# Performance work log

Measured on AMD Instinct MI355X. Metric: run time of the kernel, lower is better.

## Reference

```python
import jax, jax.numpy as jnp
import numpy as np

B, S, D, U = 8, 2048, 512, 512
L0, L1 = 128, 128  # limit_context (left, right)


def setup_inputs() -> dict:
    key = jax.random.key(0)
    ks = jax.random.split(key, 7)
    scale = 1.0 / np.sqrt(D).astype(np.float32)
    return {
        "x": jax.random.normal(ks[0], (B, S, D), dtype=jnp.float32),
        "Wq": jax.random.normal(ks[1], (D, U), dtype=jnp.float32) * scale,
        "Wk": jax.random.normal(ks[2], (D, U), dtype=jnp.float32) * scale,
        "Wv": jax.random.normal(ks[3], (D, U), dtype=jnp.float32) * scale,
        "bq": jnp.zeros((U,), dtype=jnp.float32),
        "bk": jnp.zeros((U,), dtype=jnp.float32),
        "bv": jnp.zeros((U,), dtype=jnp.float32),
    }


def reference(x, Wq, Wk, Wv, bq, bk, bv):
    # Linear projections for query / key / value (shared input x)
    q = x @ Wq + bq  # [B,S,U]
    k = x @ Wk + bk  # [B,S,U]
    v = x @ Wv + bv  # [B,S,U]

    inv_sqrt_dv = jnp.float32(1.0 / np.sqrt(U))
    scores = jnp.einsum("bqd,bkd->bqk", q, k) * inv_sqrt_dv  # [B,S,S]

    # Sliding-window mask: key j visible to query i iff i-L0 <= j <= i+L1.
    # Equivalent to the original per-step softmax over values[:, start:end].
    i = jnp.arange(S)[:, None]
    j = jnp.arange(S)[None, :]
    window = (j >= i - L0) & (j <= i + L1)  # [S,S]
    neg_inf = jnp.finfo(scores.dtype).min
    scores = jnp.where(window[None], scores, neg_inf)

    attn = jax.nn.softmax(scores, axis=-1)  # [B,S,S]
    return jnp.einsum("bqk,bkd->bqd", attn, v)  # [B,S,U]
```

## Files before the change

### kernel.cpp

```cpp
#include <hip/hip_runtime.h>

#define BATCH 8
#define S_LEN 2048
#define DDIM 512
#define UDIM 512
#define WIN_L 128
#define WIN_R 128

typedef _Float16 f16;
typedef __attribute__((ext_vector_type(8))) _Float16 f16x8;
typedef __attribute__((ext_vector_type(4))) _Float16 f16x4;
typedef __attribute__((ext_vector_type(4))) float f32x4;

__device__ __forceinline__ void gload_lds16(const void* g, void* l) {
  __builtin_amdgcn_global_load_lds((const __attribute__((address_space(1))) void*)g,
                                   (__attribute__((address_space(3))) void*)l, 16, 0, 0);
}

__global__ void cast_f32_f16(const float* __restrict__ in, f16* __restrict__ out, int n) {
  int i = (blockIdx.x * blockDim.x + threadIdx.x) * 4;
  if (i < n) {
    float4 v = *(const float4*)(in + i);
    f16x4 o;
    o[0] = (f16)v.x; o[1] = (f16)v.y; o[2] = (f16)v.z; o[3] = (f16)v.w;
    *(f16x4*)(out + i) = o;
  }
}

__global__ void transpose_w(const float* __restrict__ Wq, const float* __restrict__ Wk,
                            const float* __restrict__ Wv, f16* __restrict__ WT) {
  const float* W = blockIdx.z == 0 ? Wq : (blockIdx.z == 1 ? Wk : Wv);
  f16* WTz = WT + (size_t)blockIdx.z * DDIM * UDIM;
  __shared__ float t[32][33];
  int tx = threadIdx.x & 31, ty = threadIdx.x >> 5;
  int n0 = blockIdx.x * 32, k0 = blockIdx.y * 32;
  for (int i = 0; i < 4; i++) {
    int r = ty * 4 + i;
    t[r][tx] = W[(size_t)(k0 + r) * UDIM + n0 + tx];
  }
  __syncthreads();
  for (int i = 0; i < 4; i++) {
    int r = ty * 4 + i;
    WTz[(size_t)(n0 + r) * DDIM + k0 + tx] = (f16)t[tx][r];
  }
}

__global__ __launch_bounds__(256, 2) void gemm_qkv(
    const f16* __restrict__ X, const f16* __restrict__ WT,
    const float* __restrict__ bq, const float* __restrict__ bk, const float* __restrict__ bv,
    f16* __restrict__ QKV, f16* __restrict__ VT) {
  int z = blockIdx.z;
  const f16* WTz = WT + (size_t)z * DDIM * UDIM;
  const float* bias = z == 0 ? bq : (z == 1 ? bk : bv);
  f16* out = QKV + (size_t)z * (BATCH * S_LEN) * UDIM;

  __shared__ f16 Al[128 * 32];
  __shared__ f16 Bl[128 * 32];

  int tid = threadIdx.x, wv = tid >> 6, ln = tid & 63;
  int m0 = blockIdx.x * 128, n0 = blockIdx.y * 128;
  int wm = (wv >> 1) * 64, wn = (wv & 1) * 64;
  int lm = ln & 15, lq = ln >> 4;
  int srow = ln >> 2, scol = (ln & 3) * 8;

  f32x4 acc[4][4];
  for (int mt = 0; mt < 4; mt++)
    for (int nt = 0; nt < 4; nt++)
      for (int r = 0; r < 4; r++) acc[mt][nt][r] = 0.f;

  for (int k0 = 0; k0 < DDIM; k0 += 32) {
    for (int half = 0; half < 2; half++) {
      int r0 = half * 64 + wv * 16;
      gload_lds16(X + (size_t)(m0 + r0 + srow) * DDIM + k0 + scol, &Al[r0 * 32]);
      gload_lds16(WTz + (size_t)(n0 + r0 + srow) * DDIM + k0 + scol, &Bl[r0 * 32]);
    }
    __syncthreads();
    f16x8 af[4], bfr[4];
    for (int mt = 0; mt < 4; mt++) af[mt] = *(const f16x8*)&Al[(wm + mt * 16 + lm) * 32 + lq * 8];
    for (int nt = 0; nt < 4; nt++) bfr[nt] = *(const f16x8*)&Bl[(wn + nt * 16 + lm) * 32 + lq * 8];
    for (int mt = 0; mt < 4; mt++)
      for (int nt = 0; nt < 4; nt++)
        acc[mt][nt] = __builtin_amdgcn_mfma_f32_16x16x32_f16(af[mt], bfr[nt], acc[mt][nt], 0, 0, 0);
    __syncthreads();
  }

  if (z == 2) {
    for (int mt = 0; mt < 4; mt++)
      for (int nt = 0; nt < 4; nt++) {
        int col = n0 + wn + nt * 16 + lm;
        float bv_ = bias[col];
        int row0 = m0 + wm + mt * 16 + lq * 4;
        int bb = row0 >> 11, ss = row0 & 2047;
        f16x4 o;
        for (int r = 0; r < 4; r++) o[r] = (f16)(acc[mt][nt][r] + bv_);
        *(f16x4*)&VT[((size_t)bb * UDIM + col) * S_LEN + ss] = o;
      }
  } else {
    for (int mt = 0; mt < 4; mt++)
      for (int nt = 0; nt < 4; nt++) {
        int col = n0 + wn + nt * 16 + lm;
        float bv_ = bias[col];
        for (int r = 0; r < 4; r++) {
          int row = m0 + wm + mt * 16 + lq * 4 + r;
          out[(size_t)row * UDIM + col] = (f16)(acc[mt][nt][r] + bv_);
        }
      }
  }
}

__global__ __launch_bounds__(256, 2) void attn(
    const f16* __restrict__ Q, const f16* __restrict__ K, const f16* __restrict__ VT,
    float* __restrict__ out) {
  __shared__ float Sb[32 * 33];
  __shared__ f16 Pb[32 * 40];
  __shared__ float mrun[32], lrun[32], alph[32];

  int tid = threadIdx.x, wv = tid >> 6, ln = tid & 63;
  int lm = ln & 15, lq = ln >> 4;
  int b = blockIdx.x, q0 = blockIdx.y * 32;
  const size_t base = (size_t)b * S_LEN;

  if (tid < 32) { mrun[tid] = -INFINITY; lrun[tid] = 0.f; }

  int smt = wv >> 1, snt = wv & 1;
  f16x8 qf[16];
  {
    const f16* qrow = Q + (base + q0 + smt * 16 + lm) * (size_t)DDIM + lq * 8;
    for (int kk = 0; kk < 16; kk++) qf[kk] = *(const f16x8*)(qrow + kk * 32);
  }
  f32x4 oacc[2][8];
  for (int mt = 0; mt < 2; mt++)
    for (int nt = 0; nt < 8; nt++)
      for (int r = 0; r < 4; r++) oacc[mt][nt][r] = 0.f;

  int jlo = q0 - WIN_L; if (jlo < 0) jlo = 0;
  int jhi = q0 + 32 + WIN_R; if (jhi > S_LEN) jhi = S_LEN;

  const f16* krow = K + (base + snt * 16 + lm) * (size_t)DDIM + lq * 8;
  const f16* vrow = VT + ((size_t)b * UDIM + wv * 128 + lm) * S_LEN + lq * 8;
  const float scale = 0.044194173824159216f;

  for (int j0 = jlo; j0 < jhi; j0 += 32) {
    const f16* kp = krow + (size_t)j0 * DDIM;
    f32x4 sacc0, sacc1;
    for (int r = 0; r < 4; r++) { sacc0[r] = 0.f; sacc1[r] = 0.f; }
    for (int kk = 0; kk < 16; kk += 2) {
      f16x8 b0 = *(const f16x8*)(kp + kk * 32);
      f16x8 b1 = *(const f16x8*)(kp + (kk + 1) * 32);
      sacc0 = __builtin_amdgcn_mfma_f32_16x16x32_f16(qf[kk], b0, sacc0, 0, 0, 0);
      sacc1 = __builtin_amdgcn_mfma_f32_16x16x32_f16(qf[kk + 1], b1, sacc1, 0, 0, 0);
    }
    for (int r = 0; r < 4; r++) {
      int row = smt * 16 + lq * 4 + r;
      int col = snt * 16 + lm;
      int qi = q0 + row, kj = j0 + col;
      float v = (sacc0[r] + sacc1[r]) * scale;
      if (kj < qi - WIN_L || kj > qi + WIN_R) v = -INFINITY;
      Sb[row * 33 + col] = v;
    }
    __syncthreads();

    {
      int r = tid >> 3, l8 = tid & 7;
      float sv[4];
      float mx = -INFINITY;
      for (int cc = 0; cc < 4; cc++) {
        sv[cc] = Sb[r * 33 + l8 * 4 + cc];
        mx = fmaxf(mx, sv[cc]);
      }
      mx = fmaxf(mx, __shfl_xor(mx, 1));
      mx = fmaxf(mx, __shfl_xor(mx, 2));
      mx = fmaxf(mx, __shfl_xor(mx, 4));
      float mold = mrun[r];
      float mnew = fmaxf(mold, mx);
      float a = __expf(mold - mnew);
      float sum = 0.f;
      for (int cc = 0; cc < 4; cc++) {
        float p = __expf(sv[cc] - mnew);
        sum += p;
        Pb[r * 40 + l8 * 4 + cc] = (f16)p;
      }
      sum += __shfl_xor(sum, 1);
      sum += __shfl_xor(sum, 2);
      sum += __shfl_xor(sum, 4);
      if (l8 == 0) {
        lrun[r] = a * lrun[r] + sum;
        mrun[r] = mnew;
        alph[r] = a;
      }
    }
    __syncthreads();

    {
      float al[2][4];
      for (int mt = 0; mt < 2; mt++)
        for (int r = 0; r < 4; r++) al[mt][r] = alph[mt * 16 + lq * 4 + r];
      for (int mt = 0; mt < 2; mt++)
        for (int nt = 0; nt < 8; nt++)
          for (int r = 0; r < 4; r++) oacc[mt][nt][r] *= al[mt][r];
      f16x8 pf[2];
      for (int mt = 0; mt < 2; mt++)
        pf[mt] = *(const f16x8*)&Pb[(mt * 16 + lm) * 40 + lq * 8];
      const f16* vp = vrow + j0;
      for (int nt = 0; nt < 8; nt++) {
        f16x8 bfr = *(const f16x8*)(vp + (size_t)nt * 16 * S_LEN);
        oacc[0][nt] = __builtin_amdgcn_mfma_f32_16x16x32_f16(pf[0], bfr, oacc[0][nt], 0, 0, 0);
        oacc[1][nt] = __builtin_amdgcn_mfma_f32_16x16x32_f16(pf[1], bfr, oacc[1][nt], 0, 0, 0);
      }
    }
  }

  {
    float linv[2][4];
    for (int mt = 0; mt < 2; mt++)
      for (int r = 0; r < 4; r++) linv[mt][r] = 1.0f / lrun[mt * 16 + lq * 4 + r];
    for (int mt = 0; mt < 2; mt++)
      for (int nt = 0; nt < 8; nt++)
        for (int r = 0; r < 4; r++) {
          int row = q0 + mt * 16 + lq * 4 + r;
          int col = wv * 128 + nt * 16 + lm;
          out[(base + row) * (size_t)UDIM + col] = oacc[mt][nt][r] * linv[mt][r];
        }
  }
}

extern "C" void kernel_launch(void* const* d_in, const int* in_sizes, int n_in,
                              void* d_out, int out_size, void* d_ws, size_t ws_size,
                              hipStream_t stream) {
  const float* x  = (const float*)d_in[0];
  const float* Wq = (const float*)d_in[1];
  const float* Wk = (const float*)d_in[2];
  const float* Wv = (const float*)d_in[3];
  const float* bq = (const float*)d_in[4];
  const float* bk = (const float*)d_in[5];
  const float* bv = (const float*)d_in[6];
  float* out = (float*)d_out;

  char* ws = (char*)d_ws;
  const size_t XB_BYTES  = (size_t)BATCH * S_LEN * DDIM * 2;
  const size_t WT_BYTES  = (size_t)3 * DDIM * UDIM * 2;
  const size_t QKV_BYTES = (size_t)3 * BATCH * S_LEN * UDIM * 2;
  f16* xb  = (f16*)ws;
  f16* WT  = (f16*)(ws + XB_BYTES);
  f16* QKV = (f16*)(ws + XB_BYTES + WT_BYTES);
  f16* VT  = (f16*)(ws + XB_BYTES + WT_BYTES + QKV_BYTES);

  int n = BATCH * S_LEN * DDIM;
  cast_f32_f16<<<n / (256 * 4), 256, 0, stream>>>(x, xb, n);
  transpose_w<<<dim3(16, 16, 3), 256, 0, stream>>>(Wq, Wk, Wv, WT);
  gemm_qkv<<<dim3(128, 4, 3), 256, 0, stream>>>(xb, WT, bq, bk, bv, QKV, VT);
  attn<<<dim3(BATCH, S_LEN / 32), 256, 0, stream>>>(
      QKV, QKV + (size_t)BATCH * S_LEN * UDIM, VT, out);
}
```

Measured before the change: 188.0 us.

## Replace online softmax loop with single-pass full-window softmax in attention

The attention kernel no longer iterates over 32-key chunks with an online softmax and block barriers per chunk. It computes the whole 288-key score strip at once in registers (each wave covers 16 rows by 144 keys), does an exact max/sum reduction through two small shared arrays, writes probabilities to a single padded LDS buffer, and then runs the PV MFMAs over all 9 key steps. This removes the per-chunk barriers and rescaling, at the cost of more registers and some wasted work on clamped out-of-range keys. The QKV GEMM also now loads 64 K-values per barrier pair instead of 32, halving its sync count.

```diff
diff --git a/kernel.cpp b/kernel.cpp
--- a/kernel.cpp
+++ b/kernel.cpp
@@ -6,6 +6,7 @@
 #define UDIM 512
 #define WIN_L 128
 #define WIN_R 128
+#define PP 296
 
 typedef _Float16 f16;
 typedef __attribute__((ext_vector_type(8))) _Float16 f16x8;
@@ -54,8 +55,8 @@
   const float* bias = z == 0 ? bq : (z == 1 ? bk : bv);
   f16* out = QKV + (size_t)z * (BATCH * S_LEN) * UDIM;
 
-  __shared__ f16 Al[128 * 32];
-  __shared__ f16 Bl[128 * 32];
+  __shared__ f16 Al[2][128 * 32];
+  __shared__ f16 Bl[2][128 * 32];
 
   int tid = threadIdx.x, wv = tid >> 6, ln = tid & 63;
   int m0 = blockIdx.x * 128, n0 = blockIdx.y * 128;
@@ -68,19 +69,24 @@
     for (int nt = 0; nt < 4; nt++)
       for (int r = 0; r < 4; r++) acc[mt][nt][r] = 0.f;
 
-  for (int k0 = 0; k0 < DDIM; k0 += 32) {
+  for (int k0 = 0; k0 < DDIM; k0 += 64) {
     for (int half = 0; half < 2; half++) {
       int r0 = half * 64 + wv * 16;
-      gload_lds16(X + (size_t)(m0 + r0 + srow) * DDIM + k0 + scol, &Al[r0 * 32]);
-      gload_lds16(WTz + (size_t)(n0 + r0 + srow) * DDIM + k0 + scol, &Bl[r0 * 32]);
+      for (int c = 0; c < 2; c++) {
+        gload_lds16(X + (size_t)(m0 + r0 + srow) * DDIM + k0 + c * 32 + scol, &Al[c][r0 * 32]);
+        gload_lds16(WTz + (size_t)(n0 + r0 + srow) * DDIM + k0 + c * 32 + scol, &Bl[c][r0 * 32]);
+      }
     }
     __syncthreads();
-    f16x8 af[4], bfr[4];
-    for (int mt = 0; mt < 4; mt++) af[mt] = *(const f16x8*)&Al[(wm + mt * 16 + lm) * 32 + lq * 8];
-    for (int nt = 0; nt < 4; nt++) bfr[nt] = *(const f16x8*)&Bl[(wn + nt * 16 + lm) * 32 + lq * 8];
-    for (int mt = 0; mt < 4; mt++)
-      for (int nt = 0; nt < 4; nt++)
-        acc[mt][nt] = __builtin_amdgcn_mfma_f32_16x16x32_f16(af[mt], bfr[nt], acc[mt][nt], 0, 0, 0);
+#pragma unroll
+    for (int c = 0; c < 2; c++) {
+      f16x8 af[4], bfr[4];
+      for (int mt = 0; mt < 4; mt++) af[mt] = *(const f16x8*)&Al[c][(wm + mt * 16 + lm) * 32 + lq * 8];
+      for (int nt = 0; nt < 4; nt++) bfr[nt] = *(const f16x8*)&Bl[c][(wn + nt * 16 + lm) * 32 + lq * 8];
+      for (int mt = 0; mt < 4; mt++)
+        for (int nt = 0; nt < 4; nt++)
+          acc[mt][nt] = __builtin_amdgcn_mfma_f32_16x16x32_f16(af[mt], bfr[nt], acc[mt][nt], 0, 0, 0);
+    }
     __syncthreads();
   }
 
@@ -111,117 +117,131 @@
 __global__ __launch_bounds__(256, 2) void attn(
     const f16* __restrict__ Q, const f16* __restrict__ K, const f16* __restrict__ VT,
     float* __restrict__ out) {
-  __shared__ float Sb[32 * 33];
-  __shared__ f16 Pb[32 * 40];
-  __shared__ float mrun[32], lrun[32], alph[32];
+  __shared__ f16 Pb[32 * PP];
+  __shared__ float wmax[2][32], wsum[2][32];
 
   int tid = threadIdx.x, wv = tid >> 6, ln = tid & 63;
   int lm = ln & 15, lq = ln >> 4;
   int b = blockIdx.x, q0 = blockIdx.y * 32;
+  int rh = wv & 1, ch = wv >> 1;
   const size_t base = (size_t)b * S_LEN;
-
-  if (tid < 32) { mrun[tid] = -INFINITY; lrun[tid] = 0.f; }
-
-  int smt = wv >> 1, snt = wv & 1;
+  const int strip0 = q0 - WIN_L;
+
   f16x8 qf[16];
   {
-    const f16* qrow = Q + (base + q0 + smt * 16 + lm) * (size_t)DDIM + lq * 8;
+    const f16* qrow = Q + (base + q0 + rh * 16 + lm) * (size_t)DDIM + lq * 8;
+#pragma unroll
     for (int kk = 0; kk < 16; kk++) qf[kk] = *(const f16x8*)(qrow + kk * 32);
   }
+
+  f32x4 sacc[9];
+#pragma unroll
+  for (int t = 0; t < 9; t++)
+    for (int r = 0; r < 4; r++) sacc[t][r] = 0.f;
+#pragma unroll
+  for (int t = 0; t < 9; t++) {
+    int key = strip0 + ch * 144 + t * 16 + lm;
+    int kc = key < 0 ? 0 : (key > S_LEN - 1 ? S_LEN - 1 : key);
+    const f16* kp = K + (base + kc) * (size_t)DDIM + lq * 8;
+#pragma unroll
+    for (int kk = 0; kk < 16; kk++) {
+      f16x8 bf = *(const f16x8*)(kp + kk * 32);
+      sacc[t] = __builtin_amdgcn_mfma_f32_16x16x32_f16(qf[kk], bf, sacc[t], 0, 0, 0);
+    }
+  }
+
+  const float scale = 0.044194173824159216f;
+  float mx[4] = {-1e30f, -1e30f, -1e30f, -1e30f};
+#pragma unroll
+  for (int t = 0; t < 9; t++) {
+    int kj = strip0 + ch * 144 + t * 16 + lm;
+#pragma unroll
+    for (int r = 0; r < 4; r++) {
+      int qi = q0 + rh * 16 + lq * 4 + r;
+      float s = sacc[t][r] * scale;
+      bool ok = (kj >= 0) && (kj < S_LEN) && (kj >= qi - WIN_L) && (kj <= qi + WIN_R);
+      s = ok ? s : -1e30f;
+      sacc[t][r] = s;
+      mx[r] = fmaxf(mx[r], s);
+    }
+  }
+#pragma unroll
+  for (int r = 0; r < 4; r++) {
+    mx[r] = fmaxf(mx[r], __shfl_xor(mx[r], 1));
+    mx[r] = fmaxf(mx[r], __shfl_xor(mx[r], 2));
+    mx[r] = fmaxf(mx[r], __shfl_xor(mx[r], 4));
+    mx[r] = fmaxf(mx[r], __shfl_xor(mx[r], 8));
+  }
+  if (lm == 0) {
+#pragma unroll
+    for (int r = 0; r < 4; r++) wmax[ch][rh * 16 + lq * 4 + r] = mx[r];
+  }
+  __syncthreads();
+
+  float mrow[4], sum[4] = {0.f, 0.f, 0.f, 0.f};
+#pragma unroll
+  for (int r = 0; r < 4; r++) {
+    int row = rh * 16 + lq * 4 + r;
+    mrow[r] = fmaxf(wmax[0][row], wmax[1][row]);
+  }
+#pragma unroll
+  for (int t = 0; t < 9; t++) {
+#pragma unroll
+    for (int r = 0; r < 4; r++) {
+      float p = __expf(sacc[t][r] - mrow[r]);
+      sum[r] += p;
+      Pb[(rh * 16 + lq * 4 + r) * PP + ch * 144 + t * 16 + lm] = (f16)p;
+    }
+  }
+#pragma unroll
+  for (int r = 0; r < 4; r++) {
+    sum[r] += __shfl_xor(sum[r], 1);
+    sum[r] += __shfl_xor(sum[r], 2);
+    sum[r] += __shfl_xor(sum[r], 4);
+    sum[r] += __shfl_xor(sum[r], 8);
+  }
+  if (lm == 0) {
+#pragma unroll
+    for (int r = 0; r < 4; r++) wsum[ch][rh * 16 + lq * 4 + r] = sum[r];
+  }
+  __syncthreads();
+
   f32x4 oacc[2][8];
+#pragma unroll
   for (int mt = 0; mt < 2; mt++)
     for (int nt = 0; nt < 8; nt++)
       for (int r = 0; r < 4; r++) oacc[mt][nt][r] = 0.f;
 
-  int jlo = q0 - WIN_L; if (jlo < 0) jlo = 0;
-  int jhi = q0 + 32 + WIN_R; if (jhi > S_LEN) jhi = S_LEN;
-
-  const f16* krow = K + (base + snt * 16 + lm) * (size_t)DDIM + lq * 8;
-  const f16* vrow = VT + ((size_t)b * UDIM + wv * 128 + lm) * S_LEN + lq * 8;
-  const float scale = 0.044194173824159216f;
-
-  for (int j0 = jlo; j0 < jhi; j0 += 32) {
-    const f16* kp = krow + (size_t)j0 * DDIM;
-    f32x4 sacc0, sacc1;
-    for (int r = 0; r < 4; r++) { sacc0[r] = 0.f; sacc1[r] = 0.f; }
-    for (int kk = 0; kk < 16; kk += 2) {
-      f16x8 b0 = *(const f16x8*)(kp + kk * 32);
-      f16x8 b1 = *(const f16x8*)(kp + (kk + 1) * 32);
-      sacc0 = __builtin_amdgcn_mfma_f32_16x16x32_f16(qf[kk], b0, sacc0, 0, 0, 0);
-      sacc1 = __builtin_amdgcn_mfma_f32_16x16x32_f16(qf[kk + 1], b1, sacc1, 0, 0, 0);
-    }
+  const f16* vbase = VT + ((size_t)b * UDIM + wv * 128 + lm) * S_LEN;
+#pragma unroll
+  for (int kst = 0; kst < 9; kst++) {
+    f16x8 pf0 = *(const f16x8*)&Pb[lm * PP + kst * 32 + lq * 8];
+    f16x8 pf1 = *(const f16x8*)&Pb[(16 + lm) * PP + kst * 32 + lq * 8];
+    int key = strip0 + kst * 32 + lq * 8;
+    int kc = key < 0 ? 0 : (key > S_LEN - 8 ? S_LEN - 8 : key);
+#pragma unroll
+    for (int nt = 0; nt < 8; nt++) {
+      f16x8 vb = *(const f16x8*)(vbase + (size_t)nt * 16 * S_LEN + kc);
+      oacc[0][nt] = __builtin_amdgcn_mfma_f32_16x16x32_f16(pf0, vb, oacc[0][nt], 0, 0, 0);
+      oacc[1][nt] = __builtin_amdgcn_mfma_f32_16x16x32_f16(pf1, vb, oacc[1][nt], 0, 0, 0);
+    }
+  }
+
+  float linv[2][4];
+#pragma unroll
+  for (int mt = 0; mt < 2; mt++)
     for (int r = 0; r < 4; r++) {
-      int row = smt * 16 + lq * 4 + r;
-      int col = snt * 16 + lm;
-      int qi = q0 + row, kj = j0 + col;
-      float v = (sacc0[r] + sacc1[r]) * scale;
-      if (kj < qi - WIN_L || kj > qi + WIN_R) v = -INFINITY;
-      Sb[row * 33 + col] = v;
-    }
-    __syncthreads();
-
-    {
-      int r = tid >> 3, l8 = tid & 7;
-      float sv[4];
-      float mx = -INFINITY;
-      for (int cc = 0; cc < 4; cc++) {
-        sv[cc] = Sb[r * 33 + l8 * 4 + cc];
-        mx = fmaxf(mx, sv[cc]);
-      }
-      mx = fmaxf(mx, __shfl_xor(mx, 1));
-      mx = fmaxf(mx, __shfl_xor(mx, 2));
-      mx = fmaxf(mx, __shfl_xor(mx, 4));
-      float mold = mrun[r];
-      float mnew = fmaxf(mold, mx);
-      float a = __expf(mold - mnew);
-      float sum = 0.f;
-      for (int cc = 0; cc < 4; cc++) {
-        float p = __expf(sv[cc] - mnew);
-        sum += p;
-        Pb[r * 40 + l8 * 4 + cc] = (f16)p;
-      }
-      sum += __shfl_xor(sum, 1);
-      sum += __shfl_xor(sum, 2);
-      sum += __shfl_xor(sum, 4);
-      if (l8 == 0) {
-        lrun[r] = a * lrun[r] + sum;
-        mrun[r] = mnew;
-        alph[r] = a;
-      }
-    }
-    __syncthreads();
-
-    {
-      float al[2][4];
-      for (int mt = 0; mt < 2; mt++)
-        for (int r = 0; r < 4; r++) al[mt][r] = alph[mt * 16 + lq * 4 + r];
-      for (int mt = 0; mt < 2; mt++)
-        for (int nt = 0; nt < 8; nt++)
-          for (int r = 0; r < 4; r++) oacc[mt][nt][r] *= al[mt][r];
-      f16x8 pf[2];
-      for (int mt = 0; mt < 2; mt++)
-        pf[mt] = *(const f16x8*)&Pb[(mt * 16 + lm) * 40 + lq * 8];
-      const f16* vp = vrow + j0;
-      for (int nt = 0; nt < 8; nt++) {
-        f16x8 bfr = *(const f16x8*)(vp + (size_t)nt * 16 * S_LEN);
-        oacc[0][nt] = __builtin_amdgcn_mfma_f32_16x16x32_f16(pf[0], bfr, oacc[0][nt], 0, 0, 0);
-        oacc[1][nt] = __builtin_amdgcn_mfma_f32_16x16x32_f16(pf[1], bfr, oacc[1][nt], 0, 0, 0);
-      }
-    }
-  }
-
-  {
-    float linv[2][4];
-    for (int mt = 0; mt < 2; mt++)
-      for (int r = 0; r < 4; r++) linv[mt][r] = 1.0f / lrun[mt * 16 + lq * 4 + r];
-    for (int mt = 0; mt < 2; mt++)
-      for (int nt = 0; nt < 8; nt++)
-        for (int r = 0; r < 4; r++) {
-          int row = q0 + mt * 16 + lq * 4 + r;
-          int col = wv * 128 + nt * 16 + lm;
-          out[(base + row) * (size_t)UDIM + col] = oacc[mt][nt][r] * linv[mt][r];
-        }
-  }
+      int row = mt * 16 + lq * 4 + r;
+      linv[mt][r] = 1.0f / (wsum[0][row] + wsum[1][row]);
+    }
+#pragma unroll
+  for (int mt = 0; mt < 2; mt++)
+    for (int nt = 0; nt < 8; nt++)
+      for (int r = 0; r < 4; r++) {
+        int row = q0 + mt * 16 + lq * 4 + r;
+        int col = wv * 128 + nt * 16 + lm;
+        out[(base + row) * (size_t)UDIM + col] = oacc[mt][nt][r] * linv[mt][r];
+      }
 }
 
 extern "C" void kernel_launch(void* const* d_in, const int* in_sizes, int n_in,
```

Result: faster. 182.0 us (-3.2%).
